# Performance work log

Hardware: AMD Instinct MI355X
Metric: run time of the kernel (lower is better)

Reference implementation:

```python
import jax, jax.numpy as jnp
import numpy as np
from jax import lax

SQRT_HALF = 0.7071067811865476
LAYERS = 20
STACKS = 2
LAYERS_PER_STACK = LAYERS // STACKS
K = 3
OUT_CH = 256
RES_CH = 64
GATE_CH = 128
SKIP_CH = 256
CIN_CH = 80


def setup_inputs() -> dict:
    key = jax.random.key(0)
    ks = jax.random.split(key, 20)
    s = 0.05
    inp = {
        'x': jax.random.normal(ks[0], (4, OUT_CH, 16384), jnp.float32),
        'c': jax.random.normal(ks[1], (4, CIN_CH, 16384), jnp.float32),
        # first conv: kernel size 2 (Conv1d2x1), out_channels -> residual_channels
        'W_first': jax.random.normal(ks[2], (RES_CH, OUT_CH, 2), jnp.float32) * s,
        'b_first': jnp.zeros((RES_CH,), jnp.float32),
        # per-layer dilated conv (residual -> gate), stacked over layers
        'W_dil': jax.random.normal(ks[3], (LAYERS, GATE_CH, RES_CH, K), jnp.float32) * s,
        'b_dil': jnp.zeros((LAYERS, GATE_CH), jnp.float32),
        # per-layer local-conditioning 1x1 (cin -> gate)
        'W_c': jax.random.normal(ks[4], (LAYERS, GATE_CH, CIN_CH), jnp.float32) * s,
        'b_c': jnp.zeros((LAYERS, GATE_CH), jnp.float32),
        # per-layer 1x1 skip (gate/2 -> skip) and out (gate/2 -> residual)
        'W_skip': jax.random.normal(ks[5], (LAYERS, SKIP_CH, GATE_CH // 2), jnp.float32) * s,
        'b_skip': jnp.zeros((LAYERS, SKIP_CH), jnp.float32),
        'W_out': jax.random.normal(ks[6], (LAYERS, RES_CH, GATE_CH // 2), jnp.float32) * s,
        'b_out': jnp.zeros((LAYERS, RES_CH), jnp.float32),
        # final 1x1 convs
        'W_last1': jax.random.normal(ks[7], (SKIP_CH, SKIP_CH), jnp.float32) * s,
        'b_last1': jnp.zeros((SKIP_CH,), jnp.float32),
        'W_last2': jax.random.normal(ks[8], (OUT_CH, SKIP_CH), jnp.float32) * s,
        'b_last2': jnp.zeros((OUT_CH,), jnp.float32),
    }
    return inp


def reference(x, c, W_first, b_first, W_dil, b_dil, W_c, b_c,
              W_skip, b_skip, W_out, b_out, W_last1, b_last1, W_last2, b_last2):
    dn = ('NCH', 'OIH', 'NCH')
    # first conv: F.pad(x, (1,0)) then kernel-2 conv == causal left pad 1
    h = lax.conv_general_dilated(x, W_first, (1,), [(1, 0)], dimension_numbers=dn)
    h = jnp.tanh(h + b_first[None, :, None])  # hparams.use_tanh_embed
    skips = None
    for l in range(LAYERS):
        d = 2 ** (l % LAYERS_PER_STACK)
        # causal dilated conv: pad left (K-1)*d
        y = lax.conv_general_dilated(h, W_dil[l], (1,), [((K - 1) * d, 0)],
                                     rhs_dilation=(d,), dimension_numbers=dn)
        y = y + b_dil[l][None, :, None]
        cond = jnp.einsum('bct,gc->bgt', c, W_c[l]) + b_c[l][None, :, None]
        a, b = jnp.split(y + cond, 2, axis=1)  # gated activation units
        z = jnp.tanh(a) * jax.nn.sigmoid(b)
        s = jnp.einsum('bgt,sg->bst', z, W_skip[l]) + b_skip[l][None, :, None]
        h = (jnp.einsum('bgt,rg->brt', z, W_out[l]) + b_out[l][None, :, None] + h) * SQRT_HALF
        if skips is None:
            skips = s
        else:
            skips = (skips + s) * SQRT_HALF  # faithful to original accumulation
    out = jax.nn.relu(skips)
    out = jnp.einsum('bst,os->bot', out, W_last1) + b_last1[None, :, None]
    out = jax.nn.relu(out)
    out = jnp.einsum('bst,os->bot', out, W_last2) + b_last2[None, :, None]
    return out
```

## Files before the change

### kernel.cpp

```cpp
#include <hip/hip_runtime.h>
#include <math.h>


#define T_LEN   16384
#define NB      4
#define BT      (NB * T_LEN)
#define NLAYERS 20
#define SQH     0.70710678118654752440f

typedef _Float16 half8 __attribute__((ext_vector_type(8)));
typedef _Float16 half4 __attribute__((ext_vector_type(4)));
typedef float f32x4 __attribute__((ext_vector_type(4)));

__device__ inline f32x4 mfma16(half8 a, half8 b, f32x4 c) {
  return __builtin_amdgcn_mfma_f32_16x16x32_f16(a, b, c, 0, 0, 0);
}

__global__ __launch_bounds__(256) void prep_pack(
    const float* __restrict__ Wf, const float* __restrict__ Wdil,
    const float* __restrict__ Wc, const float* __restrict__ Wskip,
    const float* __restrict__ Wout, const float* __restrict__ Wl1,
    const float* __restrict__ Wl2, const float* __restrict__ bdil,
    const float* __restrict__ bc, const float* __restrict__ bskip,
    _Float16* __restrict__ wdp, _Float16* __restrict__ wcp,
    _Float16* __restrict__ wop, _Float16* __restrict__ wskp,
    _Float16* __restrict__ wfp, _Float16* __restrict__ wl1p,
    _Float16* __restrict__ wl2p, float* __restrict__ bde,
    float* __restrict__ bsk)
{
  const float Q = 0.70710678118654752440f;
  const int WDP_E = 20 * 3 * 128 * 64;
  const int WCP_E = 20 * 128 * 96;
  const int WOP_E = 20 * 64 * 64;
  const int WSK_E = 256 * 1280;
  const int WFP_E = 64 * 512;
  const int WL_E  = 256 * 256;
  const int BDE_E = 20 * 128;
  const int BSK_E = 256;
  const int TOTAL = WDP_E + WCP_E + WOP_E + WSK_E + WFP_E + 2 * WL_E + BDE_E + BSK_E;
  for (int i = blockIdx.x * blockDim.x + threadIdx.x; i < TOTAL;
       i += gridDim.x * blockDim.x) {
    int j = i;
    if (j < WDP_E) {
      int l = j / (3 * 128 * 64); int r2 = j % (3 * 128 * 64);
      int tau = r2 / (128 * 64);  int r3 = r2 % (128 * 64);
      int n = r3 >> 6; int kc = r3 & 63;
      wdp[j] = (_Float16)Wdil[((l * 128 + n) * 64 + kc) * 3 + tau];
      continue;
    }
    j -= WDP_E;
    if (j < WCP_E) {
      int l = j / (128 * 96); int r2 = j % (128 * 96);
      int n = r2 / 96; int kc = r2 % 96;
      wcp[j] = (_Float16)(kc < 80 ? Wc[(l * 128 + n) * 80 + kc] : 0.f);
      continue;
    }
    j -= WCP_E;
    if (j < WOP_E) {
      int l = j >> 12; int r2 = j & 4095;
      int n = r2 >> 6; int kc = r2 & 63;
      wop[j] = (_Float16)Wout[(l * 64 + n) * 64 + kc];
      continue;
    }
    j -= WOP_E;
    if (j < WSK_E) {
      int n = j / 1280; int k = j % 1280;
      int l = k >> 6; int kc = k & 63;
      float f = (l == 0) ? 1.f : powf(Q, (float)(1 - l));
      wskp[j] = (_Float16)(Wskip[(l * 256 + n) * 64 + kc] * f);
      continue;
    }
    j -= WSK_E;
    if (j < WFP_E) {
      int n = j >> 9; int k = j & 511;
      int tau = k >> 8; int ci = k & 255;
      wfp[j] = (_Float16)Wf[(n * 256 + ci) * 2 + tau];
      continue;
    }
    j -= WFP_E;
    if (j < WL_E) { wl1p[j] = (_Float16)Wl1[j]; continue; }
    j -= WL_E;
    if (j < WL_E) { wl2p[j] = (_Float16)Wl2[j]; continue; }
    j -= WL_E;
    if (j < BDE_E) { bde[j] = bdil[j] + bc[j]; continue; }
    j -= BDE_E;
    {
      int n = j;
      float s = 0.f;
      for (int l = 0; l < NLAYERS; ++l) {
        float w = powf(Q, (float)(l == 0 ? 19 : 20 - l));
        s += bskip[l * 256 + n] * w;
      }
      bsk[n] = s;
    }
  }
}

__global__ __launch_bounds__(256) void tr_kernel(
    const float* __restrict__ src, _Float16* __restrict__ dst, int C, int Cpad, int CB)
{
  __shared__ float tile[32 * 33];
  int bid = blockIdx.x;
  int cb = bid % CB;
  int tb = (bid / CB) % (T_LEN / 32);
  int bb = bid / (CB * (T_LEN / 32));
  int t0 = tb * 32, ch0 = cb * 32;
  int tl = threadIdx.x & 31, cl = threadIdx.x >> 5;
#pragma unroll
  for (int i = 0; i < 4; ++i) {
    int ch = cl + 8 * i;
    float v = (ch0 + ch < C) ? src[((size_t)bb * C + ch0 + ch) * T_LEN + t0 + tl] : 0.f;
    tile[ch * 33 + tl] = v;
  }
  __syncthreads();
  int t = threadIdx.x >> 3;
  int c4 = (threadIdx.x & 7) * 4;
  half4 hv = {(_Float16)tile[(c4 + 0) * 33 + t], (_Float16)tile[(c4 + 1) * 33 + t],
              (_Float16)tile[(c4 + 2) * 33 + t], (_Float16)tile[(c4 + 3) * 33 + t]};
  *(half4*)&dst[((size_t)bb * T_LEN + t0 + t) * Cpad + ch0 + c4] = hv;
}

__global__ __launch_bounds__(256, 4) void first_conv(
    const _Float16* __restrict__ xt, const _Float16* __restrict__ wfp,
    const float* __restrict__ bf, _Float16* __restrict__ h0)
{
  __shared__ _Float16 As[128 * 72];
  __shared__ _Float16 Bs[64 * 72];
  const int tid = threadIdx.x;
  const int lane = tid & 63, w = tid >> 6;
  const int wx = w & 1, wy = w >> 1;
  const int l15 = lane & 15, quad = lane >> 4;
  const int p0 = blockIdx.x * 128;
  const int b = p0 >> 14, t0 = p0 & (T_LEN - 1);
  const int r = tid >> 1, halfo = (tid & 1) * 32;

  f32x4 acc[4][2];
#pragma unroll
  for (int mi = 0; mi < 4; ++mi)
#pragma unroll
    for (int ni = 0; ni < 2; ++ni) { f32x4 z = {0.f, 0.f, 0.f, 0.f}; acc[mi][ni] = z; }

  for (int s = 0; s < 8; ++s) {
    int tau = s >> 2, ci0 = (s & 3) * 64;
    int ts = t0 + r - 1 + tau;
    if (ts >= 0) {
      const uint4* src = (const uint4*)(xt + ((size_t)(b * T_LEN + ts) * 256 + ci0 + halfo));
#pragma unroll
      for (int j = 0; j < 4; ++j) *(uint4*)&As[r * 72 + halfo + 8 * j] = src[j];
    } else {
      uint4 z = {0, 0, 0, 0};
#pragma unroll
      for (int j = 0; j < 4; ++j) *(uint4*)&As[r * 72 + halfo + 8 * j] = z;
    }
    if (tid < 128) {
      const uint4* s4 = (const uint4*)(wfp + ((size_t)r * 512 + tau * 256 + ci0 + halfo));
#pragma unroll
      for (int j = 0; j < 4; ++j) *(uint4*)&Bs[r * 72 + halfo + 8 * j] = s4[j];
    }
    __syncthreads();
#pragma unroll
    for (int kc = 0; kc < 2; ++kc) {
      const int k0 = kc * 32 + quad * 8;
      half8 af[4], bfr[2];
#pragma unroll
      for (int mi = 0; mi < 4; ++mi)
        af[mi] = *(const half8*)&As[(64 * wy + 16 * mi + l15) * 72 + k0];
#pragma unroll
      for (int ni = 0; ni < 2; ++ni)
        bfr[ni] = *(const half8*)&Bs[(32 * wx + 16 * ni + l15) * 72 + k0];
#pragma unroll
      for (int mi = 0; mi < 4; ++mi)
#pragma unroll
        for (int ni = 0; ni < 2; ++ni)
          acc[mi][ni] = mfma16(af[mi], bfr[ni], acc[mi][ni]);
    }
    __syncthreads();
  }
#pragma unroll
  for (int mi = 0; mi < 4; ++mi)
#pragma unroll
    for (int ni = 0; ni < 2; ++ni) {
      int col = 32 * wx + 16 * ni + l15;
      int rowb = 64 * wy + 16 * mi + quad * 4;
      float bo = bf[col];
      size_t base = ((size_t)p0 + rowb) * 64 + col;
#pragma unroll
      for (int reg = 0; reg < 4; ++reg) {
        float v = acc[mi][ni][reg] + bo;
        float e = __expf(2.f * v);
        h0[base + (size_t)64 * reg] = (_Float16)(1.f - 2.f * __builtin_amdgcn_rcpf(e + 1.f));
      }
    }
}

__global__ __launch_bounds__(512, 4) void layer_kernel(
    const _Float16* __restrict__ hprev, _Float16* __restrict__ hnext,
    const _Float16* __restrict__ ctp,
    const _Float16* __restrict__ wdp_l, const _Float16* __restrict__ wcp_l,
    const _Float16* __restrict__ wop_l,
    const float* __restrict__ bde_l, const float* __restrict__ bout_l,
    _Float16* __restrict__ zslot, int d)
{
  __shared__ _Float16 As[128 * 72];
  __shared__ _Float16 Bs[128 * 72];
  __shared__ float bde_s[128];

  const int tid = threadIdx.x;
  const int lane = tid & 63, w = tid >> 6;
  const int wx = w & 1, wy = w >> 1;
  const int l15 = lane & 15, quad = lane >> 4;
  const int p0 = blockIdx.x * 128;
  const int b = p0 >> 14, t0 = p0 & (T_LEN - 1);
  const int r2 = tid >> 2, qo = (tid & 3) * 16;
  const int o8 = (tid & 3) * 8;

  if (tid < 128) bde_s[tid] = bde_l[tid];

  f32x4 acc[2][4];
#pragma unroll
  for (int mi = 0; mi < 2; ++mi)
#pragma unroll
    for (int ni = 0; ni < 4; ++ni) { f32x4 z = {0.f, 0.f, 0.f, 0.f}; acc[mi][ni] = z; }

  for (int s = 0; s < 5; ++s) {
    if (s < 3) {
      int ts = t0 + r2 - (2 - s) * d;
      if (ts >= 0) {
        const uint4* src = (const uint4*)(hprev + ((size_t)(b * T_LEN + ts) * 64 + qo));
        *(uint4*)&As[r2 * 72 + qo] = src[0];
        *(uint4*)&As[r2 * 72 + qo + 8] = src[1];
      } else {
        uint4 z4 = {0, 0, 0, 0};
        *(uint4*)&As[r2 * 72 + qo] = z4;
        *(uint4*)&As[r2 * 72 + qo + 8] = z4;
      }
      const uint4* sb = (const uint4*)(wdp_l + ((size_t)s * 8192 + r2 * 64 + qo));
      *(uint4*)&Bs[r2 * 72 + qo] = sb[0];
      *(uint4*)&Bs[r2 * 72 + qo + 8] = sb[1];
    } else if (s == 3) {
      const uint4* sa = (const uint4*)(ctp + ((size_t)(p0 + r2) * 96 + qo));
      *(uint4*)&As[r2 * 72 + qo] = sa[0];
      *(uint4*)&As[r2 * 72 + qo + 8] = sa[1];
      const uint4* sb = (const uint4*)(wcp_l + ((size_t)r2 * 96 + qo));
      *(uint4*)&Bs[r2 * 72 + qo] = sb[0];
      *(uint4*)&Bs[r2 * 72 + qo + 8] = sb[1];
    } else {
      *(uint4*)&As[r2 * 72 + o8] = *(const uint4*)(ctp + ((size_t)(p0 + r2) * 96 + 64 + o8));
      *(uint4*)&Bs[r2 * 72 + o8] = *(const uint4*)(wcp_l + ((size_t)r2 * 96 + 64 + o8));
    }
    __syncthreads();
    const int nkc = (s == 4) ? 1 : 2;
    for (int kc = 0; kc < nkc; ++kc) {
      const int k0 = kc * 32 + quad * 8;
      half8 af[2], bfr[4];
#pragma unroll
      for (int mi = 0; mi < 2; ++mi)
        af[mi] = *(const half8*)&As[(32 * wy + 16 * mi + l15) * 72 + k0];
#pragma unroll
      for (int ni = 0; ni < 4; ++ni) {
        int ncol = 32 * wx + 16 * (ni & 1) + 64 * (ni >> 1);
        bfr[ni] = *(const half8*)&Bs[(ncol + l15) * 72 + k0];
      }
#pragma unroll
      for (int mi = 0; mi < 2; ++mi)
#pragma unroll
        for (int ni = 0; ni < 4; ++ni)
          acc[mi][ni] = mfma16(af[mi], bfr[ni], acc[mi][ni]);
    }
    __syncthreads();
  }

#pragma unroll
  for (int mi = 0; mi < 2; ++mi)
#pragma unroll
    for (int ni2 = 0; ni2 < 2; ++ni2) {
      int colb = 32 * wx + 16 * ni2 + l15;
      float ba = bde_s[colb], bb = bde_s[colb + 64];
#pragma unroll
      for (int reg = 0; reg < 4; ++reg) {
        float av = acc[mi][ni2][reg] + ba;
        float gv = acc[mi][ni2 + 2][reg] + bb;
        float ea = __expf(2.f * av);
        float th = 1.f - 2.f * __builtin_amdgcn_rcpf(ea + 1.f);
        float sg = __builtin_amdgcn_rcpf(1.f + __expf(-gv));
        As[(32 * wy + 16 * mi + quad * 4 + reg) * 72 + colb] = (_Float16)(th * sg);
      }
    }

  if (tid < 256) {
    int row = tid >> 2;
    const uint4* sb = (const uint4*)(wop_l + ((size_t)row * 64 + qo));
    *(uint4*)&Bs[row * 72 + qo] = sb[0];
    *(uint4*)&Bs[row * 72 + qo + 8] = sb[1];
  }
  __syncthreads();

  {
    uint4 v0 = *(const uint4*)&As[r2 * 72 + qo];
    uint4 v1 = *(const uint4*)&As[r2 * 72 + qo + 8];
    uint4* dst = (uint4*)(zslot + ((size_t)(p0 + r2) * 64 + qo));
    dst[0] = v0; dst[1] = v1;
  }

  f32x4 a4[2][2];
#pragma unroll
  for (int mi = 0; mi < 2; ++mi)
#pragma unroll
    for (int ni = 0; ni < 2; ++ni) { f32x4 z = {0.f, 0.f, 0.f, 0.f}; a4[mi][ni] = z; }
#pragma unroll
  for (int kc = 0; kc < 2; ++kc) {
    const int k0 = kc * 32 + quad * 8;
    half8 af[2], bfr[2];
#pragma unroll
    for (int mi = 0; mi < 2; ++mi)
      af[mi] = *(const half8*)&As[(32 * wy + 16 * mi + l15) * 72 + k0];
#pragma unroll
    for (int ni = 0; ni < 2; ++ni)
      bfr[ni] = *(const half8*)&Bs[(32 * wx + 16 * ni + l15) * 72 + k0];
#pragma unroll
    for (int mi = 0; mi < 2; ++mi)
#pragma unroll
      for (int ni = 0; ni < 2; ++ni)
        a4[mi][ni] = mfma16(af[mi], bfr[ni], a4[mi][ni]);
  }
#pragma unroll
  for (int mi = 0; mi < 2; ++mi)
#pragma unroll
    for (int ni = 0; ni < 2; ++ni) {
      int col = 32 * wx + 16 * ni + l15;
      int rowb = 32 * wy + 16 * mi + quad * 4;
      float bo = bout_l[col];
      size_t base = ((size_t)p0 + rowb) * 64 + col;
#pragma unroll
      for (int reg = 0; reg < 4; ++reg) {
        float hv = (float)hprev[base + (size_t)64 * reg];
        hnext[base + (size_t)64 * reg] = (_Float16)((a4[mi][ni][reg] + bo + hv) * SQH);
      }
    }
}

__global__ __launch_bounds__(256, 4) void flush_kernel(
    const _Float16* __restrict__ zbuf, const _Float16* __restrict__ wskp,
    _Float16* __restrict__ Abuf, const float* __restrict__ bsk,
    _Float16* __restrict__ skr, int l0, int g, int mode)
{
  __shared__ _Float16 As[128 * 72];
  __shared__ _Float16 Bs[128 * 72];
  const int tid = threadIdx.x;
  const int lane = tid & 63, w = tid >> 6;
  const int wx = w & 1, wy = w >> 1;
  const int l15 = lane & 15, quad = lane >> 4;
  const int p0 = blockIdx.x * 128;
  const int n0 = blockIdx.y * 128;
  const int r = tid >> 1, halfo = (tid & 1) * 32;

  f32x4 acc[4][4];
#pragma unroll
  for (int mi = 0; mi < 4; ++mi)
#pragma unroll
    for (int ni = 0; ni < 4; ++ni) { f32x4 z = {0.f, 0.f, 0.f, 0.f}; acc[mi][ni] = z; }

  for (int j = 0; j < g; ++j) {
    int l = l0 + j;
    const _Float16* zsl = zbuf + (size_t)(l & 7) * BT * 64;
    const uint4* sa = (const uint4*)(zsl + ((size_t)(p0 + r) * 64 + halfo));
#pragma unroll
    for (int jj = 0; jj < 4; ++jj) *(uint4*)&As[r * 72 + halfo + 8 * jj] = sa[jj];
    const uint4* sb = (const uint4*)(wskp + ((size_t)(n0 + r) * 1280 + l * 64 + halfo));
#pragma unroll
    for (int jj = 0; jj < 4; ++jj) *(uint4*)&Bs[r * 72 + halfo + 8 * jj] = sb[jj];
    __syncthreads();
#pragma unroll
    for (int kc = 0; kc < 2; ++kc) {
      const int k0 = kc * 32 + quad * 8;
      half8 af[4], bfr[4];
#pragma unroll
      for (int mi = 0; mi < 4; ++mi)
        af[mi] = *(const half8*)&As[(64 * wy + 16 * mi + l15) * 72 + k0];
#pragma unroll
      for (int ni = 0; ni < 4; ++ni)
        bfr[ni] = *(const half8*)&Bs[(64 * wx + 16 * ni + l15) * 72 + k0];
#pragma unroll
      for (int mi = 0; mi < 4; ++mi)
#pragma unroll
        for (int ni = 0; ni < 4; ++ni)
          acc[mi][ni] = mfma16(af[mi], bfr[ni], acc[mi][ni]);
    }
    __syncthreads();
  }
  const float Q19 = 0.0013810679320049757f;
#pragma unroll
  for (int mi = 0; mi < 4; ++mi)
#pragma unroll
    for (int ni = 0; ni < 4; ++ni) {
      int col = n0 + 64 * wx + 16 * ni + l15;
      int rowb = 64 * wy + 16 * mi + quad * 4;
      size_t base = ((size_t)p0 + rowb) * 256 + col;
      if (mode == 2) {
        float bb = bsk[col];
#pragma unroll
        for (int reg = 0; reg < 4; ++reg) {
          float v = (acc[mi][ni][reg] + (float)Abuf[base + (size_t)256 * reg]) * Q19 + bb;
          skr[base + (size_t)256 * reg] = (_Float16)(v > 0.f ? v : 0.f);
        }
      } else if (mode == 1) {
#pragma unroll
        for (int reg = 0; reg < 4; ++reg) {
          size_t a = base + (size_t)256 * reg;
          Abuf[a] = (_Float16)((float)Abuf[a] + acc[mi][ni][reg]);
        }
      } else {
#pragma unroll
        for (int reg = 0; reg < 4; ++reg)
          Abuf[base + (size_t)256 * reg] = (_Float16)acc[mi][ni][reg];
      }
    }
}

__global__ __launch_bounds__(256, 4) void gemm256(
    const _Float16* __restrict__ Asrc, const _Float16* __restrict__ Bp,
    const float* __restrict__ bias, void* __restrict__ dst, int mode)
{
  __shared__ _Float16 smem[2 * 128 * 72];
  _Float16* As = smem;
  _Float16* Bs = smem + 128 * 72;
  const int tid = threadIdx.x;
  const int lane = tid & 63, w = tid >> 6;
  const int wx = w & 1, wy = w >> 1;
  const int l15 = lane & 15, quad = lane >> 4;
  const int p0 = blockIdx.x * 128;
  const int n0 = blockIdx.y * 128;
  const int r = tid >> 1, halfo = (tid & 1) * 32;

  f32x4 acc[4][4];
#pragma unroll
  for (int mi = 0; mi < 4; ++mi)
#pragma unroll
    for (int ni = 0; ni < 4; ++ni) { f32x4 z = {0.f, 0.f, 0.f, 0.f}; acc[mi][ni] = z; }

  for (int c4 = 0; c4 < 4; ++c4) {
    int k0g = c4 * 64;
    const uint4* sa = (const uint4*)(Asrc + ((size_t)(p0 + r) * 256 + k0g + halfo));
#pragma unroll
    for (int jj = 0; jj < 4; ++jj) *(uint4*)&As[r * 72 + halfo + 8 * jj] = sa[jj];
    const uint4* sb = (const uint4*)(Bp + ((size_t)(n0 + r) * 256 + k0g + halfo));
#pragma unroll
    for (int jj = 0; jj < 4; ++jj) *(uint4*)&Bs[r * 72 + halfo + 8 * jj] = sb[jj];
    __syncthreads();
#pragma unroll
    for (int kc = 0; kc < 2; ++kc) {
      const int k0 = kc * 32 + quad * 8;
      half8 af[4], bfr[4];
#pragma unroll
      for (int mi = 0; mi < 4; ++mi)
        af[mi] = *(const half8*)&As[(64 * wy + 16 * mi + l15) * 72 + k0];
#pragma unroll
      for (int ni = 0; ni < 4; ++ni)
        bfr[ni] = *(const half8*)&Bs[(64 * wx + 16 * ni + l15) * 72 + k0];
#pragma unroll
      for (int mi = 0; mi < 4; ++mi)
#pragma unroll
        for (int ni = 0; ni < 4; ++ni)
          acc[mi][ni] = mfma16(af[mi], bfr[ni], acc[mi][ni]);
    }
    __syncthreads();
  }
  if (mode == 0) {
#pragma unroll
    for (int mi = 0; mi < 4; ++mi)
#pragma unroll
      for (int ni = 0; ni < 4; ++ni) {
        int col = n0 + 64 * wx + 16 * ni + l15;
        int rowb = 64 * wy + 16 * mi + quad * 4;
        float bv = bias[col];
        _Float16* o = (_Float16*)dst;
#pragma unroll
        for (int reg = 0; reg < 4; ++reg) {
          float v = acc[mi][ni][reg] + bv;
          o[((size_t)(p0 + rowb + reg)) * 256 + col] = (_Float16)(v > 0.f ? v : 0.f);
        }
      }
  } else {
    float* Ts = (float*)smem;
    const int b = p0 >> 14, t0g = p0 & (T_LEN - 1);
    for (int pass = 0; pass < 2; ++pass) {
      if (wx == pass) {
#pragma unroll
        for (int mi = 0; mi < 4; ++mi)
#pragma unroll
          for (int ni = 0; ni < 4; ++ni) {
            int col_l = 16 * ni + l15;
            float bv = bias[n0 + 64 * pass + col_l];
            int tl = 64 * wy + 16 * mi + quad * 4;
#pragma unroll
            for (int reg = 0; reg < 4; ++reg)
              Ts[col_l * 132 + tl + reg] = acc[mi][ni][reg] + bv;
          }
      }
      __syncthreads();
      {
        int col_l = tid >> 2;
        int tq = (tid & 3) * 32;
        float* o = (float*)dst + ((size_t)b * 256 + n0 + 64 * pass + col_l) * T_LEN + t0g + tq;
#pragma unroll
        for (int j = 0; j < 8; ++j)
          *(float4*)(o + 4 * j) = *(const float4*)&Ts[col_l * 132 + tq + 4 * j];
      }
      __syncthreads();
    }
  }
}

extern "C" void kernel_launch(void* const* d_in, const int* in_sizes, int n_in,
                              void* d_out, int out_size, void* d_ws, size_t ws_size,
                              hipStream_t stream)
{
  const float* x     = (const float*)d_in[0];
  const float* c     = (const float*)d_in[1];
  const float* Wf    = (const float*)d_in[2];
  const float* bf    = (const float*)d_in[3];
  const float* Wdil  = (const float*)d_in[4];
  const float* bdil  = (const float*)d_in[5];
  const float* Wc    = (const float*)d_in[6];
  const float* bc    = (const float*)d_in[7];
  const float* Wskip = (const float*)d_in[8];
  const float* bskip = (const float*)d_in[9];
  const float* Wout  = (const float*)d_in[10];
  const float* bout  = (const float*)d_in[11];
  const float* Wl1   = (const float*)d_in[12];
  const float* bl1   = (const float*)d_in[13];
  const float* Wl2   = (const float*)d_in[14];
  const float* bl2   = (const float*)d_in[15];

  char* base = (char*)d_ws;
  _Float16* zbuf = (_Float16*)base;
  _Float16* xt   = zbuf;
  _Float16* skr  = zbuf + (size_t)4 * BT * 64;
  _Float16* y1   = zbuf;
  _Float16* ctp  = (_Float16*)(base + 67108864);
  _Float16* hA   = (_Float16*)(base + 79691776);
  _Float16* hB   = (_Float16*)(base + 88080384);
  _Float16* wdp  = (_Float16*)(base + 96468992);
  _Float16* wcp  = wdp  + (size_t)20 * 3 * 128 * 64;
  _Float16* wop  = wcp  + (size_t)20 * 128 * 96;
  _Float16* wskp = wop  + (size_t)20 * 64 * 64;
  _Float16* wfp  = wskp + (size_t)256 * 1280;
  _Float16* wl1p = wfp  + (size_t)64 * 512;
  _Float16* wl2p = wl1p + (size_t)256 * 256;
  float*    bde  = (float*)(wl2p + (size_t)256 * 256);
  float*    bsk  = bde + 20 * 128;
  _Float16* Abuf = (_Float16*)d_out;

  prep_pack<<<2048, 256, 0, stream>>>(Wf, Wdil, Wc, Wskip, Wout, Wl1, Wl2,
                                      bdil, bc, bskip,
                                      wdp, wcp, wop, wskp, wfp, wl1p, wl2p,
                                      bde, bsk);
  tr_kernel<<<NB * (T_LEN / 32) * 8, 256, 0, stream>>>(x, xt, 256, 256, 8);
  tr_kernel<<<NB * (T_LEN / 32) * 3, 256, 0, stream>>>(c, ctp, 80, 96, 3);
  first_conv<<<512, 256, 0, stream>>>(xt, wfp, bf, hA);

  const _Float16* hin = hA;
  _Float16* hout = hB;
  for (int l = 0; l < NLAYERS; ++l) {
    int d = 1 << (l % 10);
    layer_kernel<<<512, 512, 0, stream>>>(
        hin, hout, ctp,
        wdp + (size_t)l * 3 * 128 * 64, wcp + (size_t)l * 128 * 96,
        wop + (size_t)l * 64 * 64, bde + l * 128, bout + l * 64,
        zbuf + (size_t)(l & 7) * BT * 64, d);
    _Float16* tmp = (_Float16*)hin; hin = hout; hout = tmp;
    if (l == 7)  flush_kernel<<<dim3(512, 2), 256, 0, stream>>>(zbuf, wskp, Abuf, bsk, skr, 0, 8, 0);
    if (l == 15) flush_kernel<<<dim3(512, 2), 256, 0, stream>>>(zbuf, wskp, Abuf, bsk, skr, 8, 8, 1);
    if (l == 19) flush_kernel<<<dim3(512, 2), 256, 0, stream>>>(zbuf, wskp, Abuf, bsk, skr, 16, 4, 2);
  }
  gemm256<<<dim3(512, 2), 256, 0, stream>>>(skr, wl1p, bl1, (void*)y1, 0);
  gemm256<<<dim3(512, 2), 256, 0, stream>>>(y1, wl2p, bl2, d_out, 1);
}
```

Baseline: 640.0 us.

## Register-prefetch next stage loads and stage residual through shared memory

```diff
diff --git a/kernel.cpp b/kernel.cpp
--- a/kernel.cpp
+++ b/kernel.cpp
@@ -199,10 +199,11 @@
     const _Float16* __restrict__ wdp_l, const _Float16* __restrict__ wcp_l,
     const _Float16* __restrict__ wop_l,
     const float* __restrict__ bde_l, const float* __restrict__ bout_l,
-    _Float16* __restrict__ zslot, int d)
+    _Float16* __restrict__ zslot, int d, int last)
 {
   __shared__ _Float16 As[128 * 72];
   __shared__ _Float16 Bs[128 * 72];
+  __shared__ _Float16 Cs[128 * 72];
   __shared__ float bde_s[128];
 
   const int tid = threadIdx.x;
@@ -222,32 +223,65 @@
 #pragma unroll
     for (int ni = 0; ni < 4; ++ni) { f32x4 z = {0.f, 0.f, 0.f, 0.f}; acc[mi][ni] = z; }
 
+  uint4 pa0, pa1, pb0, pb1;
+  bool paz = false;
+
+  auto issue = [&](int s) {
+    if (s < 3) {
+      int ts = t0 + r2 - (2 - s) * d;
+      paz = (ts < 0);
+      int tsc = paz ? 0 : ts;
+      const uint4* src = (const uint4*)(hprev + ((size_t)(b * T_LEN + tsc) * 64 + qo));
+      pa0 = src[0]; pa1 = src[1];
+      const uint4* sb = (const uint4*)(wdp_l + ((size_t)s * 8192 + r2 * 64 + qo));
+      pb0 = sb[0]; pb1 = sb[1];
+    } else if (s == 3) {
+      paz = false;
+      const uint4* sa = (const uint4*)(ctp + ((size_t)(p0 + r2) * 96 + qo));
+      pa0 = sa[0]; pa1 = sa[1];
+      const uint4* sb = (const uint4*)(wcp_l + ((size_t)r2 * 96 + qo));
+      pb0 = sb[0]; pb1 = sb[1];
+    } else {
+      paz = false;
+      pa0 = *(const uint4*)(ctp + ((size_t)(p0 + r2) * 96 + 64 + o8));
+      pb0 = *(const uint4*)(wcp_l + ((size_t)r2 * 96 + 64 + o8));
+    }
+  };
+
+  issue(0);
+#pragma unroll 1
   for (int s = 0; s < 5; ++s) {
     if (s < 3) {
-      int ts = t0 + r2 - (2 - s) * d;
-      if (ts >= 0) {
-        const uint4* src = (const uint4*)(hprev + ((size_t)(b * T_LEN + ts) * 64 + qo));
-        *(uint4*)&As[r2 * 72 + qo] = src[0];
-        *(uint4*)&As[r2 * 72 + qo + 8] = src[1];
+      if (!paz) {
+        *(uint4*)&As[r2 * 72 + qo] = pa0;
+        *(uint4*)&As[r2 * 72 + qo + 8] = pa1;
       } else {
         uint4 z4 = {0, 0, 0, 0};
         *(uint4*)&As[r2 * 72 + qo] = z4;
         *(uint4*)&As[r2 * 72 + qo + 8] = z4;
       }
-      const uint4* sb = (const uint4*)(wdp_l + ((size_t)s * 8192 + r2 * 64 + qo));
-      *(uint4*)&Bs[r2 * 72 + qo] = sb[0];
-      *(uint4*)&Bs[r2 * 72 + qo + 8] = sb[1];
+      if (s == 2) {
+        if (!paz) {
+          *(uint4*)&Cs[r2 * 72 + qo] = pa0;
+          *(uint4*)&Cs[r2 * 72 + qo + 8] = pa1;
+        } else {
+          uint4 z4 = {0, 0, 0, 0};
+          *(uint4*)&Cs[r2 * 72 + qo] = z4;
+          *(uint4*)&Cs[r2 * 72 + qo + 8] = z4;
+        }
+      }
+      *(uint4*)&Bs[r2 * 72 + qo] = pb0;
+      *(uint4*)&Bs[r2 * 72 + qo + 8] = pb1;
     } else if (s == 3) {
-      const uint4* sa = (const uint4*)(ctp + ((size_t)(p0 + r2) * 96 + qo));
-      *(uint4*)&As[r2 * 72 + qo] = sa[0];
-      *(uint4*)&As[r2 * 72 + qo + 8] = sa[1];
-      const uint4* sb = (const uint4*)(wcp_l + ((size_t)r2 * 96 + qo));
-      *(uint4*)&Bs[r2 * 72 + qo] = sb[0];
-      *(uint4*)&Bs[r2 * 72 + qo + 8] = sb[1];
+      *(uint4*)&As[r2 * 72 + qo] = pa0;
+      *(uint4*)&As[r2 * 72 + qo + 8] = pa1;
+      *(uint4*)&Bs[r2 * 72 + qo] = pb0;
+      *(uint4*)&Bs[r2 * 72 + qo + 8] = pb1;
     } else {
-      *(uint4*)&As[r2 * 72 + o8] = *(const uint4*)(ctp + ((size_t)(p0 + r2) * 96 + 64 + o8));
-      *(uint4*)&Bs[r2 * 72 + o8] = *(const uint4*)(wcp_l + ((size_t)r2 * 96 + 64 + o8));
-    }
+      *(uint4*)&As[r2 * 72 + o8] = pa0;
+      *(uint4*)&Bs[r2 * 72 + o8] = pb0;
+    }
+    if (s < 4) issue(s + 1);
     __syncthreads();
     const int nkc = (s == 4) ? 1 : 2;
     for (int kc = 0; kc < nkc; ++kc) {
@@ -287,7 +321,7 @@
       }
     }
 
-  if (tid < 256) {
+  if (!last && tid < 256) {
     int row = tid >> 2;
     const uint4* sb = (const uint4*)(wop_l + ((size_t)row * 64 + qo));
     *(uint4*)&Bs[row * 72 + qo] = sb[0];
@@ -302,6 +336,8 @@
     dst[0] = v0; dst[1] = v1;
   }
 
+  if (last) return;
+
   f32x4 a4[2][2];
 #pragma unroll
   for (int mi = 0; mi < 2; ++mi)
@@ -330,13 +366,19 @@
       int col = 32 * wx + 16 * ni + l15;
       int rowb = 32 * wy + 16 * mi + quad * 4;
       float bo = bout_l[col];
-      size_t base = ((size_t)p0 + rowb) * 64 + col;
 #pragma unroll
       for (int reg = 0; reg < 4; ++reg) {
-        float hv = (float)hprev[base + (size_t)64 * reg];
-        hnext[base + (size_t)64 * reg] = (_Float16)((a4[mi][ni][reg] + bo + hv) * SQH);
-      }
-    }
+        float hv = (float)Cs[(rowb + reg) * 72 + col];
+        Cs[(rowb + reg) * 72 + col] = (_Float16)((a4[mi][ni][reg] + bo + hv) * SQH);
+      }
+    }
+  __syncthreads();
+  {
+    uint4 v0 = *(const uint4*)&Cs[r2 * 72 + qo];
+    uint4 v1 = *(const uint4*)&Cs[r2 * 72 + qo + 8];
+    uint4* dst = (uint4*)(hnext + ((size_t)(p0 + r2) * 64 + qo));
+    dst[0] = v0; dst[1] = v1;
+  }
 }
 
 __global__ __launch_bounds__(256, 4) void flush_kernel(
@@ -360,15 +402,26 @@
 #pragma unroll
     for (int ni = 0; ni < 4; ++ni) { f32x4 z = {0.f, 0.f, 0.f, 0.f}; acc[mi][ni] = z; }
 
+  uint4 pa[4], pb[4];
+  auto issuef = [&](int j) {
+    const int lj = l0 + j;
+    const _Float16* zsl = zbuf + (size_t)(lj & 7) * ((size_t)BT * 64);
+    const uint4* sa = (const uint4*)(zsl + ((size_t)(p0 + r) * 64 + halfo));
+#pragma unroll
+    for (int jj = 0; jj < 4; ++jj) pa[jj] = sa[jj];
+    const uint4* sb = (const uint4*)(wskp + ((size_t)(n0 + r) * 1280 + lj * 64 + halfo));
+#pragma unroll
+    for (int jj = 0; jj < 4; ++jj) pb[jj] = sb[jj];
+  };
+
+  issuef(0);
+#pragma unroll 1
   for (int j = 0; j < g; ++j) {
-    int l = l0 + j;
-    const _Float16* zsl = zbuf + (size_t)(l & 7) * BT * 64;
-    const uint4* sa = (const uint4*)(zsl + ((size_t)(p0 + r) * 64 + halfo));
-#pragma unroll
-    for (int jj = 0; jj < 4; ++jj) *(uint4*)&As[r * 72 + halfo + 8 * jj] = sa[jj];
-    const uint4* sb = (const uint4*)(wskp + ((size_t)(n0 + r) * 1280 + l * 64 + halfo));
-#pragma unroll
-    for (int jj = 0; jj < 4; ++jj) *(uint4*)&Bs[r * 72 + halfo + 8 * jj] = sb[jj];
+#pragma unroll
+    for (int jj = 0; jj < 4; ++jj) *(uint4*)&As[r * 72 + halfo + 8 * jj] = pa[jj];
+#pragma unroll
+    for (int jj = 0; jj < 4; ++jj) *(uint4*)&Bs[r * 72 + halfo + 8 * jj] = pb[jj];
+    if (j + 1 < g) issuef(j + 1);
     __syncthreads();
 #pragma unroll
     for (int kc = 0; kc < 2; ++kc) {
@@ -438,14 +491,25 @@
 #pragma unroll
     for (int ni = 0; ni < 4; ++ni) { f32x4 z = {0.f, 0.f, 0.f, 0.f}; acc[mi][ni] = z; }
 
+  uint4 pa[4], pb[4];
+  auto issueg = [&](int c4) {
+    const int k0g = c4 * 64;
+    const uint4* sa = (const uint4*)(Asrc + ((size_t)(p0 + r) * 256 + k0g + halfo));
+#pragma unroll
+    for (int jj = 0; jj < 4; ++jj) pa[jj] = sa[jj];
+    const uint4* sb = (const uint4*)(Bp + ((size_t)(n0 + r) * 256 + k0g + halfo));
+#pragma unroll
+    for (int jj = 0; jj < 4; ++jj) pb[jj] = sb[jj];
+  };
+
+  issueg(0);
+#pragma unroll 1
   for (int c4 = 0; c4 < 4; ++c4) {
-    int k0g = c4 * 64;
-    const uint4* sa = (const uint4*)(Asrc + ((size_t)(p0 + r) * 256 + k0g + halfo));
-#pragma unroll
-    for (int jj = 0; jj < 4; ++jj) *(uint4*)&As[r * 72 + halfo + 8 * jj] = sa[jj];
-    const uint4* sb = (const uint4*)(Bp + ((size_t)(n0 + r) * 256 + k0g + halfo));
-#pragma unroll
-    for (int jj = 0; jj < 4; ++jj) *(uint4*)&Bs[r * 72 + halfo + 8 * jj] = sb[jj];
+#pragma unroll
+    for (int jj = 0; jj < 4; ++jj) *(uint4*)&As[r * 72 + halfo + 8 * jj] = pa[jj];
+#pragma unroll
+    for (int jj = 0; jj < 4; ++jj) *(uint4*)&Bs[r * 72 + halfo + 8 * jj] = pb[jj];
+    if (c4 < 3) issueg(c4 + 1);
     __syncthreads();
 #pragma unroll
     for (int kc = 0; kc < 2; ++kc) {
@@ -567,7 +631,7 @@
         hin, hout, ctp,
         wdp + (size_t)l * 3 * 128 * 64, wcp + (size_t)l * 128 * 96,
         wop + (size_t)l * 64 * 64, bde + l * 128, bout + l * 64,
-        zbuf + (size_t)(l & 7) * BT * 64, d);
+        zbuf + (size_t)(l & 7) * BT * 64, d, (l == NLAYERS - 1) ? 1 : 0);
     _Float16* tmp = (_Float16*)hin; hin = hout; hout = tmp;
     if (l == 7)  flush_kernel<<<dim3(512, 2), 256, 0, stream>>>(zbuf, wskp, Abuf, bsk, skr, 0, 8, 0);
     if (l == 15) flush_kernel<<<dim3(512, 2), 256, 0, stream>>>(zbuf, wskp, Abuf, bsk, skr, 8, 8, 1);
```

New measurement: 955.6 us. 49.3% more time.
